# Optimization experiments

Hardware: AMD Instinct MI355X
Metric: run time of the kernel (lower is better)

Reference implementation:

```python
import jax, jax.numpy as jnp
import numpy as np
import math

B, L, D = 2, 2048, 512
D_INNER, D_STATE, D_CONV = 2 * D, 16, 4
DT_RANK = math.ceil(D / 16)  # 32


def setup_inputs() -> dict:
    key = jax.random.key(0)
    ks = jax.random.split(key, 9)
    s = 0.02
    x = jax.random.normal(ks[0], (B, L, D), dtype=jnp.float32)
    W_in = jax.random.normal(ks[1], (D, 2 * D_INNER), dtype=jnp.float32) * s
    conv_w = jax.random.normal(ks[2], (D_INNER, D_CONV), dtype=jnp.float32) * s
    conv_b = jnp.zeros((D_INNER,), dtype=jnp.float32)
    W_x = jax.random.normal(ks[3], (D_INNER, DT_RANK + 2 * D_STATE), dtype=jnp.float32) * s
    W_dt = jax.random.normal(ks[4], (DT_RANK, D_INNER), dtype=jnp.float32) * s
    b_dt = jax.random.normal(ks[5], (D_INNER,), dtype=jnp.float32) * s
    # S4D-real init: A = -[1..d_state] per channel
    A_log = jnp.log(jnp.broadcast_to(jnp.arange(1, D_STATE + 1, dtype=jnp.float32), (D_INNER, D_STATE)))
    D_param = jnp.ones((D_INNER,), dtype=jnp.float32)
    W_out = jax.random.normal(ks[6], (D_INNER, D), dtype=jnp.float32) * s
    return {"x": x, "W_in": W_in, "conv_w": conv_w, "conv_b": conv_b,
            "W_x": W_x, "W_dt": W_dt, "b_dt": b_dt, "A_log": A_log,
            "D_param": D_param, "W_out": W_out}


def _mamba(x, W_in, conv_w, conv_b, W_x, W_dt, b_dt, A_log, D_param, W_out):
    # in_proj -> [u, z]
    xz = jnp.einsum('bld,de->ble', x, W_in)
    u, z = jnp.split(xz, 2, axis=-1)  # each (B, L, d_inner)
    # depthwise causal conv1d along L
    u_c = jnp.transpose(u, (0, 2, 1))  # (B, d_inner, L)
    kern = conv_w[:, None, :]          # (d_inner, 1, d_conv)
    u_c = jax.lax.conv_general_dilated(
        u_c, kern, window_strides=(1,), padding=[(D_CONV - 1, 0)],
        feature_group_count=D_INNER,
        dimension_numbers=('NCH', 'OIH', 'NCH')) + conv_b[None, :, None]
    u = jax.nn.silu(jnp.transpose(u_c, (0, 2, 1)))  # (B, L, d_inner)
    # input-dependent dt, B, C
    x_dbl = jnp.einsum('bld,de->ble', u, W_x)
    dt_r = x_dbl[..., :DT_RANK]
    Bm = x_dbl[..., DT_RANK:DT_RANK + D_STATE]          # (B, L, d_state)
    Cm = x_dbl[..., DT_RANK + D_STATE:]                  # (B, L, d_state)
    dt = jax.nn.softplus(jnp.einsum('blr,rd->bld', dt_r, W_dt) + b_dt)  # (B, L, d_inner)
    A = -jnp.exp(A_log)  # (d_inner, d_state)

    def step(h, inp):
        dt_t, B_t, C_t, u_t = inp  # (B,d_inner), (B,d_state), (B,d_state), (B,d_inner)
        dA = jnp.exp(dt_t[:, :, None] * A)                      # (B, d_inner, d_state)
        h = h * dA + (dt_t * u_t)[:, :, None] * B_t[:, None, :]
        y = jnp.einsum('bds,bs->bd', h, C_t)
        return h, y

    h0 = jnp.zeros((B, D_INNER, D_STATE), dtype=x.dtype)
    xs = (jnp.transpose(dt, (1, 0, 2)), jnp.transpose(Bm, (1, 0, 2)),
          jnp.transpose(Cm, (1, 0, 2)), jnp.transpose(u, (1, 0, 2)))
    _, ys = jax.lax.scan(step, h0, xs)
    y = jnp.transpose(ys, (1, 0, 2)) + u * D_param  # (B, L, d_inner)
    y = y * jax.nn.silu(z)
    return jnp.einsum('bld,de->ble', y, W_out)


def reference(x, W_in, conv_w, conv_b, W_x, W_dt, b_dt, A_log, D_param, W_out):
    # MambaLayer.forward (eval): out = x + drop_path(mamba(x)); drop_path == Identity at eval
    return x + _mamba(x, W_in, conv_w, conv_b, W_x, W_dt, b_dt, A_log, D_param, W_out)
```

## Files before the change

kernel.cpp:

```cpp
#include <hip/hip_runtime.h>
#include <math.h>

#define BB 2
#define LL 2048
#define DD 512
#define DIN 1024
#define DXZ 2048
#define DSTATE 16
#define DTRANK 32
#define NDBL 64
#define ML (BB*LL)
#define LC3 32
#define NCH3 64
#define CP3 36
#define PHS 17

typedef __bf16 bf16_t;
typedef bf16_t bf16x8 __attribute__((ext_vector_type(8)));
typedef bf16_t bf16x4 __attribute__((ext_vector_type(4)));
typedef float f32x4 __attribute__((ext_vector_type(4)));

#define GBK 32
#define GBKP 40

__device__ __forceinline__ float fast_silu(float x) {
  return x * __builtin_amdgcn_rcpf(1.f + __builtin_amdgcn_exp2f(-1.44269504f * x));
}

template <int TM, int TN, int MODE, int CT>
__launch_bounds__(256)
__global__ void gemm_mfma(const bf16_t* __restrict__ A,
                          const bf16_t* __restrict__ Bt,
                          float* __restrict__ C, int ldc,
                          int M, int N, int K,
                          const float* __restrict__ aux) {
  __shared__ __align__(16) bf16_t As[TM * GBKP];
  __shared__ __align__(16) bf16_t Bs[TN * GBKP];
  const int tid = threadIdx.x;
  const int wid = tid >> 6, lane = tid & 63;
  const int q = lane >> 4, ln = lane & 15;
  constexpr int WM = TM / 2, WN = TN / 2;
  constexpr int FM = WM / 16, FN = WN / 16;
  const int wm = (wid >> 1) * WM, wn = (wid & 1) * WN;
  const int mBase = blockIdx.y * TM, nBase = blockIdx.x * TN;

  f32x4 acc[FM][FN] = {};

  for (int k0 = 0; k0 < K; k0 += GBK) {
#pragma unroll
    for (int i = 0; i < TM * GBK / (256 * 8); i++) {
      const int slot = tid + i * 256;
      const int m = slot >> 2, k8 = (slot & 3) * 8;
      *(bf16x8*)&As[m * GBKP + k8] =
          *(const bf16x8*)&A[(size_t)(mBase + m) * K + k0 + k8];
    }
#pragma unroll
    for (int i = 0; i < TN * GBK / (256 * 8); i++) {
      const int slot = tid + i * 256;
      const int n = slot >> 2, k8 = (slot & 3) * 8;
      *(bf16x8*)&Bs[n * GBKP + k8] =
          *(const bf16x8*)&Bt[(size_t)(nBase + n) * K + k0 + k8];
    }
    __syncthreads();
    bf16x8 af[FM], bfr[FN];
#pragma unroll
    for (int i = 0; i < FM; i++)
      af[i] = *(const bf16x8*)&As[(wm + i * 16 + ln) * GBKP + q * 8];
#pragma unroll
    for (int j = 0; j < FN; j++)
      bfr[j] = *(const bf16x8*)&Bs[(wn + j * 16 + ln) * GBKP + q * 8];
#pragma unroll
    for (int i = 0; i < FM; i++)
#pragma unroll
      for (int j = 0; j < FN; j++)
        acc[i][j] = __builtin_amdgcn_mfma_f32_16x16x32_bf16(
            af[i], bfr[j], acc[i][j], 0, 0, 0);
    __syncthreads();
  }

#pragma unroll
  for (int i = 0; i < FM; i++) {
    const int m0 = mBase + wm + i * 16 + q * 4;
#pragma unroll
    for (int j = 0; j < FN; j++) {
      const int n = nBase + wn + j * 16 + ln;
      if (CT == 1) {
        *(f32x4*)&C[(size_t)n * ldc + m0] = acc[i][j];
      } else {
#pragma unroll
        for (int r = 0; r < 4; r++) {
          float v = acc[i][j][r];
          if (MODE == 2) v += aux[(size_t)(m0 + r) * ldc + n];
          C[(size_t)(m0 + r) * ldc + n] = v;
        }
      }
    }
  }
}

__global__ void cast_bf16(const float* __restrict__ in, bf16_t* __restrict__ out,
                          int n4) {
  const int i = blockIdx.x * 256 + threadIdx.x;
  if (i >= n4) return;
  const float4 v = ((const float4*)in)[i];
  bf16x4 o = {(bf16_t)v.x, (bf16_t)v.y, (bf16_t)v.z, (bf16_t)v.w};
  ((bf16x4*)out)[i] = o;
}

__launch_bounds__(256)
__global__ void transpose_cast(const float* __restrict__ in, bf16_t* __restrict__ out,
                               int R, int C) {
  __shared__ float T[64][65];
  const int t = threadIdx.x;
  const int rB = blockIdx.y * 64, cB = blockIdx.x * 64;
  {
    const int r = t >> 4, c4 = (t & 15) * 4;
#pragma unroll
    for (int i = 0; i < 4; i++) {
      const float4 v = *(const float4*)&in[(size_t)(rB + r + i * 16) * C + cB + c4];
      T[r + i * 16][c4] = v.x;
      T[r + i * 16][c4 + 1] = v.y;
      T[r + i * 16][c4 + 2] = v.z;
      T[r + i * 16][c4 + 3] = v.w;
    }
  }
  __syncthreads();
  {
    const int c = t >> 2;
#pragma unroll
    for (int i = 0; i < 4; i++) {
      const int r0 = (t & 3) * 16 + i * 4;
      bf16x4 o = {(bf16_t)T[r0][c], (bf16_t)T[r0 + 1][c],
                  (bf16_t)T[r0 + 2][c], (bf16_t)T[r0 + 3][c]};
      *(bf16x4*)&out[(size_t)(cB + c) * R + rB + r0] = o;
    }
  }
}

template <int MODE, int AT, int CT>
__launch_bounds__(256)
__global__ void gemm_tiled(const float* __restrict__ A, int lda,
                           const float* __restrict__ B, int ldb,
                           float* __restrict__ C, int ldc,
                           int M, int N, int K,
                           const float* __restrict__ aux) {
  __shared__ float As[16][68];
  __shared__ float Bs[16][68];

  const int tid = threadIdx.x;
  const int tx = tid & 15, ty = tid >> 4;
  const int mBase = blockIdx.y * 64;
  const int nBase = blockIdx.x * 64;

  float acc[4][4] = {};

  for (int k0 = 0; k0 < K; k0 += 16) {
#pragma unroll
    for (int i = 0; i < 4; i++) {
      int idx = tid + i * 256;
      if (AT == 0) {
        int m = idx >> 4, kk = idx & 15;
        As[kk][m] = A[(size_t)(mBase + m) * lda + k0 + kk];
      } else {
        int kk = idx >> 6, m = idx & 63;
        As[kk][m] = A[(size_t)(k0 + kk) * lda + mBase + m];
      }
    }
#pragma unroll
    for (int i = 0; i < 4; i++) {
      int idx = tid + i * 256;
      int kk = idx >> 6, n = idx & 63;
      Bs[kk][n] = B[(size_t)(k0 + kk) * ldb + nBase + n];
    }
    __syncthreads();
#pragma unroll
    for (int kk = 0; kk < 16; kk++) {
      const float4 a4 = *reinterpret_cast<const float4*>(&As[kk][ty * 4]);
      const float4 b4 = *reinterpret_cast<const float4*>(&Bs[kk][tx * 4]);
      const float a[4] = {a4.x, a4.y, a4.z, a4.w};
      const float b[4] = {b4.x, b4.y, b4.z, b4.w};
#pragma unroll
      for (int i = 0; i < 4; i++)
#pragma unroll
        for (int j = 0; j < 4; j++) acc[i][j] = fmaf(a[i], b[j], acc[i][j]);
    }
    __syncthreads();
  }

  if (CT == 0) {
#pragma unroll
    for (int i = 0; i < 4; i++) {
      const int m = mBase + ty * 4 + i;
      const int n0 = nBase + tx * 4;
      float v[4];
#pragma unroll
      for (int j = 0; j < 4; j++) {
        float x = acc[i][j];
        if (MODE == 1) {
          x += aux[n0 + j];
          x = (x > 20.f) ? x
              : 0.69314718f * __builtin_amdgcn_logf(
                    1.f + __builtin_amdgcn_exp2f(x * 1.44269504f));
        }
        v[j] = x;
      }
      *reinterpret_cast<float4*>(&C[(size_t)m * ldc + n0]) =
          make_float4(v[0], v[1], v[2], v[3]);
    }
  } else {
    const int m0 = mBase + ty * 4;
#pragma unroll
    for (int j = 0; j < 4; j++) {
      const int n = nBase + tx * 4 + j;
      float v[4];
#pragma unroll
      for (int i = 0; i < 4; i++) {
        float x = acc[i][j];
        if (MODE == 1) {
          x += aux[n];
          x = (x > 20.f) ? x
              : 0.69314718f * __builtin_amdgcn_logf(
                    1.f + __builtin_amdgcn_exp2f(x * 1.44269504f));
        }
        v[i] = x;
      }
      *reinterpret_cast<float4*>(&C[(size_t)n * ldc + m0]) =
          make_float4(v[0], v[1], v[2], v[3]);
    }
  }
}

__launch_bounds__(256)
__global__ void conv_silu_T(const float* __restrict__ xzT,
                            const float* __restrict__ conv_w,
                            const float* __restrict__ conv_b,
                            float* __restrict__ uT) {
  const int idx = blockIdx.x * 256 + threadIdx.x;
  const int d = idx >> 10;
  const int ml0 = (idx & 1023) * 4;
  const int l0 = ml0 & (LL - 1);
  const float* row = xzT + (size_t)d * ML + ml0;
  const float4 Bv = *reinterpret_cast<const float4*>(row);
  float4 Av = make_float4(0.f, 0.f, 0.f, 0.f);
  if (l0 != 0) Av = *reinterpret_cast<const float4*>(row - 4);
  const float w0 = conv_w[d * 4 + 0], w1 = conv_w[d * 4 + 1];
  const float w2 = conv_w[d * 4 + 2], w3 = conv_w[d * 4 + 3];
  const float bias = conv_b[d];
  float o[4];
  o[0] = bias + w0 * Av.y + w1 * Av.z + w2 * Av.w + w3 * Bv.x;
  o[1] = bias + w0 * Av.z + w1 * Av.w + w2 * Bv.x + w3 * Bv.y;
  o[2] = bias + w0 * Av.w + w1 * Bv.x + w2 * Bv.y + w3 * Bv.z;
  o[3] = bias + w0 * Bv.x + w1 * Bv.y + w2 * Bv.z + w3 * Bv.w;
#pragma unroll
  for (int i = 0; i < 4; i++) o[i] = fast_silu(o[i]);
  *reinterpret_cast<float4*>(uT + (size_t)d * ML + ml0) =
      make_float4(o[0], o[1], o[2], o[3]);
}

__launch_bounds__(256, 4)
__global__ void scan_fused6(const float* __restrict__ dtT,
                            const float* __restrict__ uT,
                            float* __restrict__ xzT,
                            const float* __restrict__ xdbl,
                            const float* __restrict__ A_log,
                            const float* __restrict__ D_param) {
  __shared__ float dt_s[NCH3 * CP3];
  __shared__ float u_s[NCH3 * CP3];
  __shared__ float Pc[NCH3][PHS];
  __shared__ float Hc[NCH3][PHS];

  const int tid = threadIdx.x;
  const int c = blockIdx.x;
  const int b = c >> 10, d = c & (DIN - 1);
  const size_t rowoff = (size_t)d * ML + (size_t)b * LL;
  const float* dtrow = dtT + rowoff;
  const float* urow  = uT + rowoff;
  const float* zrow  = xzT + (size_t)(DIN + d) * ML + (size_t)b * LL;
  float* yrow = xzT + rowoff;

#pragma unroll
  for (int i = 0; i < 2; i++) {
    const int idx = (tid + i * 256) * 4;
    const int la = (idx >> 5) * CP3 + (idx & 31);
    *(float4*)&dt_s[la] = *(const float4*)&dtrow[idx];
    *(float4*)&u_s[la]  = *(const float4*)&urow[idx];
  }

  const int ch = tid >> 2, q = tid & 3;
  const int s0 = q * 4;
  float Al2[4];
#pragma unroll
  for (int k = 0; k < 4; k++)
    Al2[k] = -expf(A_log[d * DSTATE + s0 + k]) * 1.44269504f;
  const float* dp = dt_s + ch * CP3;
  float* up = u_s + ch * CP3;
  const float* BC = xdbl + ((size_t)b * LL + (size_t)ch * LC3) * NDBL + DTRANK + s0;
  __syncthreads();

  {
    float h0 = 0.f, h1 = 0.f, h2 = 0.f, h3 = 0.f, sdt = 0.f;
    float4 Bcur[4];
#pragma unroll
    for (int i = 0; i < 4; i++)
      Bcur[i] = *(const float4*)(BC + (size_t)i * NDBL);
    for (int g = 0; g < 8; g++) {
      float4 Bnxt[4];
#pragma unroll
      for (int i = 0; i < 4; i++)
        Bnxt[i] = *(const float4*)(BC + (size_t)((g + 1) * 4 + i) * NDBL);
#pragma unroll
      for (int i = 0; i < 4; i++) {
        const int l = g * 4 + i;
        const float dtv = dp[l];
        const float dtu = dtv * up[l];
        sdt += dtv;
        const float e0 = __builtin_amdgcn_exp2f(dtv * Al2[0]);
        const float e1 = __builtin_amdgcn_exp2f(dtv * Al2[1]);
        const float e2 = __builtin_amdgcn_exp2f(dtv * Al2[2]);
        const float e3 = __builtin_amdgcn_exp2f(dtv * Al2[3]);
        h0 = fmaf(h0, e0, dtu * Bcur[i].x);
        h1 = fmaf(h1, e1, dtu * Bcur[i].y);
        h2 = fmaf(h2, e2, dtu * Bcur[i].z);
        h3 = fmaf(h3, e3, dtu * Bcur[i].w);
      }
#pragma unroll
      for (int i = 0; i < 4; i++) Bcur[i] = Bnxt[i];
    }
    Pc[ch][s0 + 0] = __builtin_amdgcn_exp2f(Al2[0] * sdt);
    Pc[ch][s0 + 1] = __builtin_amdgcn_exp2f(Al2[1] * sdt);
    Pc[ch][s0 + 2] = __builtin_amdgcn_exp2f(Al2[2] * sdt);
    Pc[ch][s0 + 3] = __builtin_amdgcn_exp2f(Al2[3] * sdt);
    Hc[ch][s0 + 0] = h0;
    Hc[ch][s0 + 1] = h1;
    Hc[ch][s0 + 2] = h2;
    Hc[ch][s0 + 3] = h3;
  }
  __syncthreads();

  if (tid < DSTATE) {
    float h = 0.f;
#pragma unroll
    for (int k = 0; k < NCH3; k++) {
      const float Pv = Pc[k][tid], Hv = Hc[k][tid];
      Pc[k][tid] = h;
      h = fmaf(h, Pv, Hv);
    }
  }
  __syncthreads();

  {
    const float Dp = D_param[d];
    float h0 = Pc[ch][s0], h1 = Pc[ch][s0 + 1];
    float h2 = Pc[ch][s0 + 2], h3 = Pc[ch][s0 + 3];
    float4 Bcur[4], Ccur[4];
#pragma unroll
    for (int i = 0; i < 4; i++) {
      Bcur[i] = *(const float4*)(BC + (size_t)i * NDBL);
      Ccur[i] = *(const float4*)(BC + (size_t)i * NDBL + DSTATE);
    }
    for (int g = 0; g < 8; g++) {
      float4 Bnxt[4], Cnxt[4];
#pragma unroll
      for (int i = 0; i < 4; i++) {
        Bnxt[i] = *(const float4*)(BC + (size_t)((g + 1) * 4 + i) * NDBL);
        Cnxt[i] = *(const float4*)(BC + (size_t)((g + 1) * 4 + i) * NDBL + DSTATE);
      }
#pragma unroll
      for (int i = 0; i < 4; i++) {
        const int l = g * 4 + i;
        const float dtv = dp[l];
        const float uv = up[l];
        const float dtu = dtv * uv;
        const float e0 = __builtin_amdgcn_exp2f(dtv * Al2[0]);
        const float e1 = __builtin_amdgcn_exp2f(dtv * Al2[1]);
        const float e2 = __builtin_amdgcn_exp2f(dtv * Al2[2]);
        const float e3 = __builtin_amdgcn_exp2f(dtv * Al2[3]);
        h0 = fmaf(h0, e0, dtu * Bcur[i].x);
        h1 = fmaf(h1, e1, dtu * Bcur[i].y);
        h2 = fmaf(h2, e2, dtu * Bcur[i].z);
        h3 = fmaf(h3, e3, dtu * Bcur[i].w);
        float p = fmaf(h0, Ccur[i].x,
                  fmaf(h1, Ccur[i].y, fmaf(h2, Ccur[i].z, h3 * Ccur[i].w)));
        p += __int_as_float(__builtin_amdgcn_ds_swizzle(__float_as_int(p), 0x041F));
        p += __int_as_float(__builtin_amdgcn_ds_swizzle(__float_as_int(p), 0x081F));
        if (q == (l & 3)) up[l] = fmaf(uv, Dp, p);
      }
#pragma unroll
      for (int i = 0; i < 4; i++) { Bcur[i] = Bnxt[i]; Ccur[i] = Cnxt[i]; }
    }
  }
  __syncthreads();

#pragma unroll
  for (int i = 0; i < 2; i++) {
    const int idx = (tid + i * 256) * 4;
    const int la = (idx >> 5) * CP3 + (idx & 31);
    const float4 y4 = *(const float4*)&u_s[la];
    const float4 z4 = *(const float4*)&zrow[idx];
    float4 o;
    o.x = y4.x * fast_silu(z4.x);
    o.y = y4.y * fast_silu(z4.y);
    o.z = y4.z * fast_silu(z4.z);
    o.w = y4.w * fast_silu(z4.w);
    *(float4*)&yrow[idx] = o;
  }
}

extern "C" void kernel_launch(void* const* d_in, const int* in_sizes, int n_in,
                              void* d_out, int out_size, void* d_ws, size_t ws_size,
                              hipStream_t stream) {
  const float* x      = (const float*)d_in[0];
  const float* W_in   = (const float*)d_in[1];
  const float* conv_w = (const float*)d_in[2];
  const float* conv_b = (const float*)d_in[3];
  const float* W_x    = (const float*)d_in[4];
  const float* W_dt   = (const float*)d_in[5];
  const float* b_dt   = (const float*)d_in[6];
  const float* A_log  = (const float*)d_in[7];
  const float* D_par  = (const float*)d_in[8];
  const float* W_out  = (const float*)d_in[9];
  float* out = (float*)d_out;

  char* ws = (char*)d_ws;
  float* xzT   = (float*)(ws);
  float* uT    = (float*)(ws + (size_t)ML * DXZ * 4);
  float* x_dbl = (float*)(ws + (size_t)ML * (DXZ + DIN) * 4);
  char* dtT_b  = ws + (size_t)ML * (DXZ + DIN + NDBL) * 4;
  float* dtT   = (float*)dtT_b;
  bf16_t* u_b  = (bf16_t*)dtT_b;
  bf16_t* y_b  = (bf16_t*)(dtT_b + (size_t)ML * DIN * 2);
  char* extra  = ws + (size_t)ML * (DXZ + DIN + NDBL + DIN) * 4;
  bf16_t* x_b      = (bf16_t*)(extra);
  bf16_t* W_inT_b  = (bf16_t*)(extra + (size_t)ML * DD * 2);
  bf16_t* W_outT_b = (bf16_t*)(extra + (size_t)ML * DD * 2 + (size_t)DXZ * DD * 2);
  bf16_t* W_xT_b   = (bf16_t*)(extra + (size_t)ML * DD * 2 + (size_t)DXZ * DD * 2
                               + (size_t)DD * DIN * 2);

  cast_bf16<<<(ML * DD / 4) / 256, 256, 0, stream>>>(x, x_b, ML * DD / 4);
  transpose_cast<<<dim3(DXZ / 64, DD / 64), 256, 0, stream>>>(W_in, W_inT_b, DD, DXZ);
  transpose_cast<<<dim3(1, DIN / 64), 256, 0, stream>>>(W_x, W_xT_b, DIN, NDBL);
  transpose_cast<<<dim3(DD / 64, DIN / 64), 256, 0, stream>>>(W_out, W_outT_b, DIN, DD);

  gemm_mfma<128, 128, 0, 1><<<dim3(DXZ / 128, ML / 128), 256, 0, stream>>>(
      x_b, W_inT_b, xzT, ML, ML, DXZ, DD, nullptr);

  conv_silu_T<<<(DIN * (ML / 4)) / 256, 256, 0, stream>>>(xzT, conv_w, conv_b, uT);

  transpose_cast<<<dim3(ML / 64, DIN / 64), 256, 0, stream>>>(uT, u_b, DIN, ML);

  gemm_mfma<64, 64, 0, 0><<<dim3(1, ML / 64), 256, 0, stream>>>(
      u_b, W_xT_b, x_dbl, NDBL, ML, NDBL, DIN, nullptr);

  gemm_tiled<1, 0, 1><<<dim3(DIN / 64, ML / 64), 256, 0, stream>>>(
      x_dbl, NDBL, W_dt, DIN, dtT, ML, ML, DIN, DTRANK, b_dt);

  scan_fused6<<<BB * DIN, 256, 0, stream>>>(dtT, uT, xzT, x_dbl, A_log, D_par);

  transpose_cast<<<dim3(ML / 64, DIN / 64), 256, 0, stream>>>(xzT, y_b, DIN, ML);

  gemm_mfma<128, 64, 2, 0><<<dim3(DD / 64, ML / 128), 256, 0, stream>>>(
      y_b, W_outT_b, out, DD, ML, DD, DIN, x);
}
```

Measured before the change: 224.8 us.

## Replace two-pass chunked scan with single pass plus carry-in correction

The chunked selective scan used to run the recurrence twice, once for chunk-end states and once for outputs starting from carried-in states. It now runs once from a zero state, emitting partial outputs and saving the running sum of dt per step. After the cross-chunk prefix, a cheap correction adds C·(H_in·exp(A·cumsum dt)) to each output. This removes the serial first pass but adds 16 exp2 per output element in the correction, plus extra registers and shared-memory traffic.

```diff
diff --git a/kernel.cpp b/kernel.cpp
--- a/kernel.cpp
+++ b/kernel.cpp
@@ -258,7 +258,7 @@
 }
 
 __launch_bounds__(256, 4)
-__global__ void scan_fused6(const float* __restrict__ dtT,
+__global__ void scan_fused7(const float* __restrict__ dtT,
                             const float* __restrict__ uT,
                             float* __restrict__ xzT,
                             const float* __restrict__ xdbl,
@@ -268,6 +268,7 @@
   __shared__ float u_s[NCH3 * CP3];
   __shared__ float Pc[NCH3][PHS];
   __shared__ float Hc[NCH3][PHS];
+  __shared__ float Al2v[DSTATE];
 
   const int tid = threadIdx.x;
   const int c = blockIdx.x;
@@ -278,6 +279,9 @@
   const float* zrow  = xzT + (size_t)(DIN + d) * ML + (size_t)b * LL;
   float* yrow = xzT + rowoff;
 
+  if (tid < DSTATE)
+    Al2v[tid] = -expf(A_log[d * DSTATE + tid]) * 1.44269504f;
+
 #pragma unroll
   for (int i = 0; i < 2; i++) {
     const int idx = (tid + i * 256) * 4;
@@ -288,70 +292,20 @@
 
   const int ch = tid >> 2, q = tid & 3;
   const int s0 = q * 4;
+  const float* dp = dt_s + ch * CP3;
+  float* dpw = dt_s + ch * CP3;
+  float* up = u_s + ch * CP3;
+  const float* BC0 = xdbl + ((size_t)b * LL + (size_t)ch * LC3) * NDBL + DTRANK;
+  const float* BC = BC0 + s0;
+  __syncthreads();
+
   float Al2[4];
 #pragma unroll
-  for (int k = 0; k < 4; k++)
-    Al2[k] = -expf(A_log[d * DSTATE + s0 + k]) * 1.44269504f;
-  const float* dp = dt_s + ch * CP3;
-  float* up = u_s + ch * CP3;
-  const float* BC = xdbl + ((size_t)b * LL + (size_t)ch * LC3) * NDBL + DTRANK + s0;
-  __syncthreads();
-
-  {
-    float h0 = 0.f, h1 = 0.f, h2 = 0.f, h3 = 0.f, sdt = 0.f;
-    float4 Bcur[4];
-#pragma unroll
-    for (int i = 0; i < 4; i++)
-      Bcur[i] = *(const float4*)(BC + (size_t)i * NDBL);
-    for (int g = 0; g < 8; g++) {
-      float4 Bnxt[4];
-#pragma unroll
-      for (int i = 0; i < 4; i++)
-        Bnxt[i] = *(const float4*)(BC + (size_t)((g + 1) * 4 + i) * NDBL);
-#pragma unroll
-      for (int i = 0; i < 4; i++) {
-        const int l = g * 4 + i;
-        const float dtv = dp[l];
-        const float dtu = dtv * up[l];
-        sdt += dtv;
-        const float e0 = __builtin_amdgcn_exp2f(dtv * Al2[0]);
-        const float e1 = __builtin_amdgcn_exp2f(dtv * Al2[1]);
-        const float e2 = __builtin_amdgcn_exp2f(dtv * Al2[2]);
-        const float e3 = __builtin_amdgcn_exp2f(dtv * Al2[3]);
-        h0 = fmaf(h0, e0, dtu * Bcur[i].x);
-        h1 = fmaf(h1, e1, dtu * Bcur[i].y);
-        h2 = fmaf(h2, e2, dtu * Bcur[i].z);
-        h3 = fmaf(h3, e3, dtu * Bcur[i].w);
-      }
-#pragma unroll
-      for (int i = 0; i < 4; i++) Bcur[i] = Bnxt[i];
-    }
-    Pc[ch][s0 + 0] = __builtin_amdgcn_exp2f(Al2[0] * sdt);
-    Pc[ch][s0 + 1] = __builtin_amdgcn_exp2f(Al2[1] * sdt);
-    Pc[ch][s0 + 2] = __builtin_amdgcn_exp2f(Al2[2] * sdt);
-    Pc[ch][s0 + 3] = __builtin_amdgcn_exp2f(Al2[3] * sdt);
-    Hc[ch][s0 + 0] = h0;
-    Hc[ch][s0 + 1] = h1;
-    Hc[ch][s0 + 2] = h2;
-    Hc[ch][s0 + 3] = h3;
-  }
-  __syncthreads();
-
-  if (tid < DSTATE) {
-    float h = 0.f;
-#pragma unroll
-    for (int k = 0; k < NCH3; k++) {
-      const float Pv = Pc[k][tid], Hv = Hc[k][tid];
-      Pc[k][tid] = h;
-      h = fmaf(h, Pv, Hv);
-    }
-  }
-  __syncthreads();
+  for (int k = 0; k < 4; k++) Al2[k] = Al2v[s0 + k];
 
   {
     const float Dp = D_param[d];
-    float h0 = Pc[ch][s0], h1 = Pc[ch][s0 + 1];
-    float h2 = Pc[ch][s0 + 2], h3 = Pc[ch][s0 + 3];
+    float h0 = 0.f, h1 = 0.f, h2 = 0.f, h3 = 0.f, sdt = 0.f;
     float4 Bcur[4], Ccur[4];
 #pragma unroll
     for (int i = 0; i < 4; i++) {
@@ -371,6 +325,7 @@
         const float dtv = dp[l];
         const float uv = up[l];
         const float dtu = dtv * uv;
+        sdt += dtv;
         const float e0 = __builtin_amdgcn_exp2f(dtv * Al2[0]);
         const float e1 = __builtin_amdgcn_exp2f(dtv * Al2[1]);
         const float e2 = __builtin_amdgcn_exp2f(dtv * Al2[2]);
@@ -383,10 +338,71 @@
                   fmaf(h1, Ccur[i].y, fmaf(h2, Ccur[i].z, h3 * Ccur[i].w)));
         p += __int_as_float(__builtin_amdgcn_ds_swizzle(__float_as_int(p), 0x041F));
         p += __int_as_float(__builtin_amdgcn_ds_swizzle(__float_as_int(p), 0x081F));
-        if (q == (l & 3)) up[l] = fmaf(uv, Dp, p);
+        if (q == i) {
+          up[l] = fmaf(uv, Dp, p);
+          dpw[l] = sdt;
+        }
       }
 #pragma unroll
       for (int i = 0; i < 4; i++) { Bcur[i] = Bnxt[i]; Ccur[i] = Cnxt[i]; }
+    }
+    Pc[ch][s0 + 0] = __builtin_amdgcn_exp2f(Al2[0] * sdt);
+    Pc[ch][s0 + 1] = __builtin_amdgcn_exp2f(Al2[1] * sdt);
+    Pc[ch][s0 + 2] = __builtin_amdgcn_exp2f(Al2[2] * sdt);
+    Pc[ch][s0 + 3] = __builtin_amdgcn_exp2f(Al2[3] * sdt);
+    Hc[ch][s0 + 0] = h0;
+    Hc[ch][s0 + 1] = h1;
+    Hc[ch][s0 + 2] = h2;
+    Hc[ch][s0 + 3] = h3;
+  }
+  __syncthreads();
+
+  if (tid < DSTATE) {
+    float h = 0.f;
+#pragma unroll
+    for (int k = 0; k < NCH3; k++) {
+      const float Pv = Pc[k][tid], Hv = Hc[k][tid];
+      Pc[k][tid] = h;
+      h = fmaf(h, Pv, Hv);
+    }
+  }
+  __syncthreads();
+
+  {
+    float Hin[16], Af[16];
+#pragma unroll
+    for (int s = 0; s < 16; s++) {
+      Hin[s] = Pc[ch][s];
+      Af[s] = Al2v[s];
+    }
+#pragma unroll
+    for (int j = 0; j < 8; j++) {
+      const int l = q + j * 4;
+      const float S = dp[l];
+      const float yl = up[l];
+      const float* Cl = BC0 + (size_t)l * NDBL + DSTATE;
+      const float4 C0 = *(const float4*)(Cl);
+      const float4 C1 = *(const float4*)(Cl + 4);
+      const float4 C2 = *(const float4*)(Cl + 8);
+      const float4 C3 = *(const float4*)(Cl + 12);
+      float pa = yl, pb = 0.f, pcc = 0.f, pd = 0.f;
+      pa  = fmaf(Hin[0]  * __builtin_amdgcn_exp2f(Af[0]  * S), C0.x, pa);
+      pb  = fmaf(Hin[1]  * __builtin_amdgcn_exp2f(Af[1]  * S), C0.y, pb);
+      pcc = fmaf(Hin[2]  * __builtin_amdgcn_exp2f(Af[2]  * S), C0.z, pcc);
+      pd  = fmaf(Hin[3]  * __builtin_amdgcn_exp2f(Af[3]  * S), C0.w, pd);
+      pa  = fmaf(Hin[4]  * __builtin_amdgcn_exp2f(Af[4]  * S), C1.x, pa);
+      pb  = fmaf(Hin[5]  * __builtin_amdgcn_exp2f(Af[5]  * S), C1.y, pb);
+      pcc = fmaf(Hin[6]  * __builtin_amdgcn_exp2f(Af[6]  * S), C1.z, pcc);
+      pd  = fmaf(Hin[7]  * __builtin_amdgcn_exp2f(Af[7]  * S), C1.w, pd);
+      pa  = fmaf(Hin[8]  * __builtin_amdgcn_exp2f(Af[8]  * S), C2.x, pa);
+      pb  = fmaf(Hin[9]  * __builtin_amdgcn_exp2f(Af[9]  * S), C2.y, pb);
+      pcc = fmaf(Hin[10] * __builtin_amdgcn_exp2f(Af[10] * S), C2.z, pcc);
+      pd  = fmaf(Hin[11] * __builtin_amdgcn_exp2f(Af[11] * S), C2.w, pd);
+      pa  = fmaf(Hin[12] * __builtin_amdgcn_exp2f(Af[12] * S), C3.x, pa);
+      pb  = fmaf(Hin[13] * __builtin_amdgcn_exp2f(Af[13] * S), C3.y, pb);
+      pcc = fmaf(Hin[14] * __builtin_amdgcn_exp2f(Af[14] * S), C3.z, pcc);
+      pd  = fmaf(Hin[15] * __builtin_amdgcn_exp2f(Af[15] * S), C3.w, pd);
+      up[l] = (pa + pb) + (pcc + pd);
     }
   }
   __syncthreads();
@@ -454,7 +470,7 @@
   gemm_tiled<1, 0, 1><<<dim3(DIN / 64, ML / 64), 256, 0, stream>>>(
       x_dbl, NDBL, W_dt, DIN, dtT, ML, ML, DIN, DTRANK, b_dt);
 
-  scan_fused6<<<BB * DIN, 256, 0, stream>>>(dtT, uT, xzT, x_dbl, A_log, D_par);
+  scan_fused7<<<BB * DIN, 256, 0, stream>>>(dtT, uT, xzT, x_dbl, A_log, D_par);
 
   transpose_cast<<<dim3(ML / 64, DIN / 64), 256, 0, stream>>>(xzT, y_b, DIN, ML);
 
```

After: 233.4 us. 3.9% more time.

## Use direct global-to-LDS loads in MFMA GEMM and fuse conv with transpose-cast

Applied to the files above, without the earlier changes.

The GEMM tile loads now use the global_load_lds builtin to move bf16 data straight into shared memory, bypassing registers, and drop the padded LDS row stride. Separately, the depthwise conv+SiLU kernel is merged with the following transpose-to-bf16 kernel, writing both the fp32 output and the transposed bf16 copy through an LDS tile. This removes one kernel launch and a full re-read of uT. Without padding, the MFMA fragment reads from LDS may hit more bank conflicts.

```diff
diff --git a/kernel.cpp b/kernel.cpp
--- a/kernel.cpp
+++ b/kernel.cpp
@@ -21,7 +21,9 @@
 typedef float f32x4 __attribute__((ext_vector_type(4)));
 
 #define GBK 32
-#define GBKP 40
+
+typedef const __attribute__((address_space(1))) void* gp1_t;
+typedef __attribute__((address_space(3))) void* lp3_t;
 
 __device__ __forceinline__ float fast_silu(float x) {
   return x * __builtin_amdgcn_rcpf(1.f + __builtin_amdgcn_exp2f(-1.44269504f * x));
@@ -34,41 +36,44 @@
                           float* __restrict__ C, int ldc,
                           int M, int N, int K,
                           const float* __restrict__ aux) {
-  __shared__ __align__(16) bf16_t As[TM * GBKP];
-  __shared__ __align__(16) bf16_t Bs[TN * GBKP];
+  __shared__ __align__(16) bf16_t As[TM * GBK];
+  __shared__ __align__(16) bf16_t Bs[TN * GBK];
   const int tid = threadIdx.x;
   const int wid = tid >> 6, lane = tid & 63;
   const int q = lane >> 4, ln = lane & 15;
   constexpr int WM = TM / 2, WN = TN / 2;
   constexpr int FM = WM / 16, FN = WN / 16;
+  constexpr int AI = TM / 64;
+  constexpr int BI = TN / 64;
   const int wm = (wid >> 1) * WM, wn = (wid & 1) * WN;
   const int mBase = blockIdx.y * TM, nBase = blockIdx.x * TN;
+  const int lr = lane >> 2, lk = (lane & 3) * 8;
 
   f32x4 acc[FM][FN] = {};
 
   for (int k0 = 0; k0 < K; k0 += GBK) {
 #pragma unroll
-    for (int i = 0; i < TM * GBK / (256 * 8); i++) {
-      const int slot = tid + i * 256;
-      const int m = slot >> 2, k8 = (slot & 3) * 8;
-      *(bf16x8*)&As[m * GBKP + k8] =
-          *(const bf16x8*)&A[(size_t)(mBase + m) * K + k0 + k8];
-    }
-#pragma unroll
-    for (int i = 0; i < TN * GBK / (256 * 8); i++) {
-      const int slot = tid + i * 256;
-      const int n = slot >> 2, k8 = (slot & 3) * 8;
-      *(bf16x8*)&Bs[n * GBKP + k8] =
-          *(const bf16x8*)&Bt[(size_t)(nBase + n) * K + k0 + k8];
+    for (int t = 0; t < AI; t++) {
+      const int grp = wid * AI + t;
+      const bf16_t* g = &A[(size_t)(mBase + grp * 16 + lr) * K + k0 + lk];
+      __builtin_amdgcn_global_load_lds((gp1_t)(const void*)g,
+                                       (lp3_t)(void*)&As[grp * 512], 16, 0, 0);
+    }
+#pragma unroll
+    for (int t = 0; t < BI; t++) {
+      const int grp = wid * BI + t;
+      const bf16_t* g = &Bt[(size_t)(nBase + grp * 16 + lr) * K + k0 + lk];
+      __builtin_amdgcn_global_load_lds((gp1_t)(const void*)g,
+                                       (lp3_t)(void*)&Bs[grp * 512], 16, 0, 0);
     }
     __syncthreads();
     bf16x8 af[FM], bfr[FN];
 #pragma unroll
     for (int i = 0; i < FM; i++)
-      af[i] = *(const bf16x8*)&As[(wm + i * 16 + ln) * GBKP + q * 8];
+      af[i] = *(const bf16x8*)&As[(wm + i * 16 + ln) * GBK + q * 8];
 #pragma unroll
     for (int j = 0; j < FN; j++)
-      bfr[j] = *(const bf16x8*)&Bs[(wn + j * 16 + ln) * GBKP + q * 8];
+      bfr[j] = *(const bf16x8*)&Bs[(wn + j * 16 + ln) * GBK + q * 8];
 #pragma unroll
     for (int i = 0; i < FM; i++)
 #pragma unroll
@@ -231,30 +236,51 @@
 }
 
 __launch_bounds__(256)
-__global__ void conv_silu_T(const float* __restrict__ xzT,
-                            const float* __restrict__ conv_w,
-                            const float* __restrict__ conv_b,
-                            float* __restrict__ uT) {
-  const int idx = blockIdx.x * 256 + threadIdx.x;
-  const int d = idx >> 10;
-  const int ml0 = (idx & 1023) * 4;
-  const int l0 = ml0 & (LL - 1);
-  const float* row = xzT + (size_t)d * ML + ml0;
-  const float4 Bv = *reinterpret_cast<const float4*>(row);
-  float4 Av = make_float4(0.f, 0.f, 0.f, 0.f);
-  if (l0 != 0) Av = *reinterpret_cast<const float4*>(row - 4);
+__global__ void conv_silu_T2(const float* __restrict__ xzT,
+                             const float* __restrict__ conv_w,
+                             const float* __restrict__ conv_b,
+                             float* __restrict__ uT,
+                             bf16_t* __restrict__ u_b) {
+  __shared__ bf16_t T[64][72];
+  const int t = threadIdx.x;
+  const int d0 = blockIdx.y * 64, ml0 = blockIdx.x * 64;
+  const int dd = t >> 2;
+  const int m4 = (t & 3) * 16;
+  const int d = d0 + dd;
+  const float* row = xzT + (size_t)d * ML + ml0 + m4;
+  float* orow = uT + (size_t)d * ML + ml0 + m4;
   const float w0 = conv_w[d * 4 + 0], w1 = conv_w[d * 4 + 1];
   const float w2 = conv_w[d * 4 + 2], w3 = conv_w[d * 4 + 3];
   const float bias = conv_b[d];
-  float o[4];
-  o[0] = bias + w0 * Av.y + w1 * Av.z + w2 * Av.w + w3 * Bv.x;
-  o[1] = bias + w0 * Av.z + w1 * Av.w + w2 * Bv.x + w3 * Bv.y;
-  o[2] = bias + w0 * Av.w + w1 * Bv.x + w2 * Bv.y + w3 * Bv.z;
-  o[3] = bias + w0 * Bv.x + w1 * Bv.y + w2 * Bv.z + w3 * Bv.w;
-#pragma unroll
-  for (int i = 0; i < 4; i++) o[i] = fast_silu(o[i]);
-  *reinterpret_cast<float4*>(uT + (size_t)d * ML + ml0) =
-      make_float4(o[0], o[1], o[2], o[3]);
+  const int l0 = (ml0 + m4) & (LL - 1);
+  float4 Av = make_float4(0.f, 0.f, 0.f, 0.f);
+  if (l0 != 0) Av = *(const float4*)(row - 4);
+#pragma unroll
+  for (int j = 0; j < 4; j++) {
+    const float4 Bv = *(const float4*)(row + j * 4);
+    float o0 = bias + w0 * Av.y + w1 * Av.z + w2 * Av.w + w3 * Bv.x;
+    float o1 = bias + w0 * Av.z + w1 * Av.w + w2 * Bv.x + w3 * Bv.y;
+    float o2 = bias + w0 * Av.w + w1 * Bv.x + w2 * Bv.y + w3 * Bv.z;
+    float o3 = bias + w0 * Bv.x + w1 * Bv.y + w2 * Bv.z + w3 * Bv.w;
+    o0 = fast_silu(o0); o1 = fast_silu(o1);
+    o2 = fast_silu(o2); o3 = fast_silu(o3);
+    *(float4*)(orow + j * 4) = make_float4(o0, o1, o2, o3);
+    T[m4 + j * 4 + 0][dd] = (bf16_t)o0;
+    T[m4 + j * 4 + 1][dd] = (bf16_t)o1;
+    T[m4 + j * 4 + 2][dd] = (bf16_t)o2;
+    T[m4 + j * 4 + 3][dd] = (bf16_t)o3;
+    Av = Bv;
+  }
+  __syncthreads();
+  const int r = t >> 2;
+#pragma unroll
+  for (int i = 0; i < 2; i++) {
+    const int cc = (t & 3) * 16 + i * 8;
+    bf16x8 v;
+#pragma unroll
+    for (int k = 0; k < 8; k++) v[k] = T[r][cc + k];
+    *(bf16x8*)&u_b[(size_t)(ml0 + r) * DIN + d0 + cc] = v;
+  }
 }
 
 __launch_bounds__(256, 4)
@@ -444,9 +470,8 @@
   gemm_mfma<128, 128, 0, 1><<<dim3(DXZ / 128, ML / 128), 256, 0, stream>>>(
       x_b, W_inT_b, xzT, ML, ML, DXZ, DD, nullptr);
 
-  conv_silu_T<<<(DIN * (ML / 4)) / 256, 256, 0, stream>>>(xzT, conv_w, conv_b, uT);
-
-  transpose_cast<<<dim3(ML / 64, DIN / 64), 256, 0, stream>>>(uT, u_b, DIN, ML);
+  conv_silu_T2<<<dim3(ML / 64, DIN / 64), 256, 0, stream>>>(
+      xzT, conv_w, conv_b, uT, u_b);
 
   gemm_mfma<64, 64, 0, 0><<<dim3(1, ML / 64), 256, 0, stream>>>(
       u_b, W_xT_b, x_dbl, NDBL, ML, NDBL, DIN, nullptr);
```

Measured after the change: 218.1 us. -3.0%, faster.
